# Kernel tuning notes

Hardware: AMD Instinct MI355X
Metric: run time of the kernel (lower is better)

Reference implementation:

```python
import jax, jax.numpy as jnp
import numpy as np

B, T, C, H = 2, 2048, 1024, 16
D = C // H  # head_dim = 64


def setup_inputs() -> dict:
    key = jax.random.key(0)
    ks = jax.random.split(key, 5)
    s = 1.0 / np.sqrt(C)
    return {
        "x": jax.random.normal(ks[0], (B, T, C), jnp.float32),
        "Wq": jax.random.normal(ks[1], (C, C), jnp.float32) * s,
        "bq": jnp.zeros((C,), jnp.float32),
        "Wk": jax.random.normal(ks[2], (C, C), jnp.float32) * s,
        "bk": jnp.zeros((C,), jnp.float32),
        "Wv": jax.random.normal(ks[3], (C, C), jnp.float32) * s,
        "bv": jnp.zeros((C,), jnp.float32),
        "Wo": jax.random.normal(ks[4], (C, C), jnp.float32) * s,
        "bo": jnp.zeros((C,), jnp.float32),
    }


def reference(x, Wq, bq, Wk, bk, Wv, bv, Wo, bo):
    Bx, Tx, Cx = x.shape
    # torch Linear: y = x @ W.T + b
    q = (x @ Wq.T + bq).reshape(Bx, Tx, H, D).transpose(0, 2, 1, 3)  # [B,H,T,D]
    k = (x @ Wk.T + bk).reshape(Bx, Tx, H, D).transpose(0, 2, 1, 3)
    v = (x @ Wv.T + bv).reshape(Bx, Tx, H, D).transpose(0, 2, 1, 3)
    att = jnp.einsum("bhqd,bhkd->bhqk", q, k) / np.sqrt(D).astype(np.float32)
    mask = jnp.tril(jnp.ones((Tx, Tx), bool))  # causal mask [T,T]
    att = jnp.where(mask, att, -jnp.inf)
    att = jax.nn.softmax(att, axis=-1)
    out = jnp.einsum("bhqk,bhkd->bhqd", att, v)
    out = out.transpose(0, 2, 1, 3).reshape(Bx, Tx, Cx)
    return out @ Wo.T + bo
```

## Files before the change

kernel.cpp:

```cpp
#include <hip/hip_runtime.h>
#include <hip/hip_bf16.h>

#define B_ 2
#define T_ 2048
#define C_ 1024
#define H_ 16
#define D_ 64

typedef unsigned short u16;
typedef __bf16 bf16x8 __attribute__((ext_vector_type(8)));
typedef float floatx4 __attribute__((ext_vector_type(4)));

__device__ __forceinline__ float bf2f(u16 u) {
  union { unsigned int i; float f; } x; x.i = ((unsigned int)u) << 16; return x.f;
}
__device__ __forceinline__ u16 f2bf(float f) {
  union { float f; unsigned int i; } x; x.f = f;
  unsigned int r = x.i + 0x7fffu + ((x.i >> 16) & 1u);
  return (u16)(r >> 16);
}

__device__ __forceinline__ unsigned cvtpk(float lo, float hi) {
  unsigned r;
  asm("v_cvt_pk_bf16_f32 %0, %1, %2" : "=v"(r) : "v"(lo), "v"(hi));
  return r;
}

__device__ __forceinline__ void gld16(void* lds, const void* g) {
  __builtin_amdgcn_global_load_lds(
      (const __attribute__((address_space(1))) unsigned int*)g,
      (__attribute__((address_space(3))) unsigned int*)lds, 16, 0, 0);
}

#define NXF4 1048576
#define NWF4 262144

__global__ __launch_bounds__(256) void cvt_all(
    const float* __restrict__ x,  const float* __restrict__ Wq,
    const float* __restrict__ Wk, const float* __restrict__ Wv,
    const float* __restrict__ Wo, u16* __restrict__ dst_base)
{
  const int i = blockIdx.x * 256 + threadIdx.x;
  const float* src; size_t off;
  if (i < NXF4)               { src = x;  off = i; }
  else if (i < NXF4 + NWF4)   { src = Wq; off = i - NXF4; }
  else if (i < NXF4 + 2*NWF4) { src = Wk; off = i - (NXF4 + NWF4); }
  else if (i < NXF4 + 3*NWF4) { src = Wv; off = i - (NXF4 + 2*NWF4); }
  else                        { src = Wo; off = i - (NXF4 + 3*NWF4); }
  float4 f = ((const float4*)src)[off];
  ushort4 o;
  o.x = f2bf(f.x); o.y = f2bf(f.y); o.z = f2bf(f.z); o.w = f2bf(f.w);
  ((ushort4*)dst_base)[i] = o;
}

#define QSCALE 0.1803368801111f

#define PBAR()                                                \
  do {                                                        \
    asm volatile("" ::: "memory");                            \
    __builtin_amdgcn_s_barrier();                             \
    asm volatile("s_waitcnt lgkmcnt(0)" ::: "memory");        \
  } while (0)

#define EBAR()                                                \
  do {                                                        \
    asm volatile("" ::: "memory");                            \
    __builtin_amdgcn_s_barrier();                             \
    asm volatile("" ::: "memory");                            \
  } while (0)

__global__ __launch_bounds__(512, 2) void gemm_qkv8(
    const u16* __restrict__ X, const u16* __restrict__ Wb,
    const float* __restrict__ b0, const float* __restrict__ b1,
    const float* __restrict__ b2,
    u16* __restrict__ Yq, u16* __restrict__ Yk, u16* __restrict__ Yv)
{
  __shared__ __align__(16) u16 L[57344];

  const int tid  = threadIdx.x;
  const int lane = tid & 63;
  const int m16  = lane & 15;
  const int q4   = lane >> 4;
  const int wv   = tid >> 6;
  const int wm   = wv >> 2;
  const int wn   = wv & 3;

  const int bid = blockIdx.x;
  const int xcd = bid & 7;
  const int idx = bid >> 3;
  const int bx  = (xcd & 3) * 4 + (idx & 3);
  const int by  = (xcd >> 2) * 8 + (idx >> 2);

  const u16* Abase  = X  + (size_t)bx * 256 * C_;
  const u16* Bbase  = Wb + (size_t)by * 192 * C_;
  const u16* A1base = Abase + (size_t)128 * C_;

  const int rB  = tid >> 3;
  const int s0 = tid,       r0 = rB;
  const int s1 = tid + 512, r1 = 64 + rB;
  const int k0a = ((tid & 7) ^ (rB & 7)) * 8;

#define STAGE_A(dsthalf, srcrows, kofs)                                       \
  do {                                                                        \
    gld16(&(dsthalf)[s0 * 8], (srcrows) + (size_t)r0 * C_ + (kofs) + k0a);    \
    gld16(&(dsthalf)[s1 * 8], (srcrows) + (size_t)r1 * C_ + (kofs) + k0a);    \
  } while (0)

#define STAGE_BL(dstB, srcrows, kofs, l)                                      \
  gld16(&(dstB)[((l) * 512 + tid) * 8],                                       \
        (srcrows) + (size_t)((l) * 64 + rB) * C_ + (kofs) + k0a)

  u16* buf0 = L;
  u16* buf1 = L + 28672;

  STAGE_BL(buf0 + 16384, Bbase, 0, 0);
  STAGE_BL(buf0 + 16384, Bbase, 0, 1);
  STAGE_BL(buf0 + 16384, Bbase, 0, 2);
  STAGE_A (buf0,         Abase,  0);
  STAGE_A (buf0 + 8192,  A1base, 0);
  STAGE_BL(buf1 + 16384, Bbase, 64, 0);
  STAGE_BL(buf1 + 16384, Bbase, 64, 1);
  STAGE_A (buf1,         Abase, 64);
  asm volatile("s_waitcnt vmcnt(4)" ::: "memory");
  __builtin_amdgcn_s_barrier();
  asm volatile("" ::: "memory");

  floatx4 acc[8][3] = {};

  const int a0off = m16 * 64 + ((q4      ^ (lane & 7)) * 8);
  const int a1off = m16 * 64 + (((q4 + 4) ^ (lane & 7)) * 8);
  const int bro   = wn * 3072;

  for (int i = 0; i < 16; ++i) {
    u16* buf  = (i & 1) ? buf1 : buf0;
    u16* bufn = (i & 1) ? buf0 : buf1;
    const u16* Ah = buf + wm * 8192;
    const u16* Bh = buf + 16384;
    const bool p1 = (i + 1) < 16;
    const bool p2 = (i + 2) < 16;
    const int  k1 = (i + 1) * 64;
    const int  k2 = (i + 2) * 64;

    bf16x8 a[4][2], bA[2][2], bB[2];

#pragma unroll
    for (int f = 0; f < 4; ++f) {
      a[f][0] = *(const bf16x8*)&Ah[f * 1024 + a0off];
      a[f][1] = *(const bf16x8*)&Ah[f * 1024 + a1off];
    }
#pragma unroll
    for (int g = 0; g < 2; ++g) {
      bA[g][0] = *(const bf16x8*)&Bh[bro + g * 1024 + a0off];
      bA[g][1] = *(const bf16x8*)&Bh[bro + g * 1024 + a1off];
    }
    if (p1) STAGE_A(bufn + 8192, A1base, k1);
    PBAR();
    __builtin_amdgcn_s_setprio(1);
#pragma unroll
    for (int f = 0; f < 4; ++f)
#pragma unroll
      for (int g = 0; g < 2; ++g) {
        acc[f][g] = __builtin_amdgcn_mfma_f32_16x16x32_bf16(a[f][0], bA[g][0], acc[f][g], 0, 0, 0);
        acc[f][g] = __builtin_amdgcn_mfma_f32_16x16x32_bf16(a[f][1], bA[g][1], acc[f][g], 0, 0, 0);
      }
    __builtin_amdgcn_s_setprio(0);
    EBAR();

    bB[0] = *(const bf16x8*)&Bh[bro + 2048 + a0off];
    bB[1] = *(const bf16x8*)&Bh[bro + 2048 + a1off];
    if (p1) STAGE_BL(bufn + 16384, Bbase, k1, 2);
    PBAR();
    __builtin_amdgcn_s_setprio(1);
#pragma unroll
    for (int f = 0; f < 4; ++f) {
      acc[f][2] = __builtin_amdgcn_mfma_f32_16x16x32_bf16(a[f][0], bB[0], acc[f][2], 0, 0, 0);
      acc[f][2] = __builtin_amdgcn_mfma_f32_16x16x32_bf16(a[f][1], bB[1], acc[f][2], 0, 0, 0);
    }
    __builtin_amdgcn_s_setprio(0);
    EBAR();

#pragma unroll
    for (int f = 0; f < 4; ++f) {
      a[f][0] = *(const bf16x8*)&Ah[4096 + f * 1024 + a0off];
      a[f][1] = *(const bf16x8*)&Ah[4096 + f * 1024 + a1off];
    }
    if (p2) {
      STAGE_BL(buf + 16384, Bbase, k2, 0);
      STAGE_BL(buf + 16384, Bbase, k2, 1);
    }
    PBAR();
    __builtin_amdgcn_s_setprio(1);
#pragma unroll
    for (int f = 0; f < 4; ++f) {
      acc[4 + f][2] = __builtin_amdgcn_mfma_f32_16x16x32_bf16(a[f][0], bB[0], acc[4 + f][2], 0, 0, 0);
      acc[4 + f][2] = __builtin_amdgcn_mfma_f32_16x16x32_bf16(a[f][1], bB[1], acc[4 + f][2], 0, 0, 0);
    }
    __builtin_amdgcn_s_setprio(0);
    EBAR();

    if (p2) STAGE_A(buf, Abase, k2);
    PBAR();
    __builtin_amdgcn_s_setprio(1);
#pragma unroll
    for (int f = 0; f < 4; ++f)
#pragma unroll
      for (int g = 0; g < 2; ++g) {
        acc[4 + f][g] = __builtin_amdgcn_mfma_f32_16x16x32_bf16(a[f][0], bA[g][0], acc[4 + f][g], 0, 0, 0);
        acc[4 + f][g] = __builtin_amdgcn_mfma_f32_16x16x32_bf16(a[f][1], bA[g][1], acc[4 + f][g], 0, 0, 0);
      }
    __builtin_amdgcn_s_setprio(0);
    asm volatile("" ::: "memory");
    if (p2) asm volatile("s_waitcnt vmcnt(4)" ::: "memory");
    else    asm volatile("s_waitcnt vmcnt(0)" ::: "memory");
    __builtin_amdgcn_s_barrier();
    asm volatile("" ::: "memory");
  }

  const int mbase = bx * 256 + wm * 128 + q4 * 4;
#pragma unroll
  for (int nf = 0; nf < 3; ++nf) {
    const int nzg = by * 192 + wn * 48 + nf * 16 + m16;
    const int z  = nzg >> 10;
    const int nl = nzg & 1023;
    if (z == 2) {
      const int h = nl >> 6, d = nl & (D_ - 1);
      const float bv = b2[nl];
#pragma unroll
      for (int mf = 0; mf < 8; ++mf) {
        const int m  = mbase + mf * 16;
        const int bb = m >> 11, t = m & (T_ - 1);
        ushort4 pk;
        pk.x = f2bf(acc[mf][nf][0] + bv);
        pk.y = f2bf(acc[mf][nf][1] + bv);
        pk.z = f2bf(acc[mf][nf][2] + bv);
        pk.w = f2bf(acc[mf][nf][3] + bv);
        *(ushort4*)&Yv[(((size_t)bb * H_ + h) * D_ + d) * T_ + t] = pk;
      }
    } else {
      const float bv = (z == 0 ? b0 : b1)[nl];
      const float sc = z ? 1.0f : QSCALE;
      const int c_loc = wn * 48 + nf * 16 + m16;
      const int chunk = c_loc >> 3, cl = c_loc & 7;
#pragma unroll
      for (int mf = 0; mf < 8; ++mf) {
#pragma unroll
        for (int r = 0; r < 4; ++r) {
          const int t_loc = wm * 128 + mf * 16 + q4 * 4 + r;
          const int pc = ((chunk & ~7) | ((chunk & 7) ^ (t_loc & 7))) * 8 + cl;
          L[t_loc * 192 + pc] = f2bf((acc[mf][nf][r] + bv) * sc);
        }
      }
    }
  }
  __syncthreads();
  {
    const int row_off = tid >> 3;
    const int ch_off  = tid & 7;
#pragma unroll
    for (int gi = 0; gi < 3; ++gi) {
      const int gg = by * 3 + gi;
      const int z  = gg >> 4;
      if (z == 2) continue;
      u16* Y = z ? Yk : Yq;
      const int h = gg & 15;
#pragma unroll
      for (int pass = 0; pass < 4; ++pass) {
        const int t_loc = pass * 64 + row_off;
        const int pl3 = ch_off ^ (t_loc & 7);
        const uint4 val = *(const uint4*)&L[t_loc * 192 + (gi * 8 + pl3) * 8];
        const int m = bx * 256 + t_loc;
        const int bb = m >> 11, tq = m & (T_ - 1);
        *(uint4*)&Y[(((size_t)bb * H_ + h) * T_ + tq) * D_ + ch_off * 8] = val;
      }
    }
  }
}

__global__ __launch_bounds__(256) void gemm_out(
    const u16* __restrict__ X, const u16* __restrict__ W,
    const float* __restrict__ bias, float* __restrict__ Yf)
{
  const int K = C_, N = C_;
  __shared__ __align__(16) u16 As[128 * 32];
  __shared__ __align__(16) u16 Bs[128 * 32];

  const int tid  = threadIdx.x;
  const int wv   = tid >> 6;
  const int lane = tid & 63;
  const int mcol = lane & 15;
  const int quad = lane >> 4;
  const int wr = wv >> 1, wc = wv & 1;
  const int m0 = blockIdx.x * 128;
  const int n0 = blockIdx.y * 128;

  const int srow = tid >> 2;
  const int scol = (tid & 3) * 8;
  const u16* xp0 = X + (size_t)(m0 + srow) * K + scol;
  const u16* xp1 = xp0 + (size_t)64 * K;
  const u16* wp0 = W + (size_t)(n0 + srow) * K + scol;
  const u16* wp1 = wp0 + (size_t)64 * K;

  floatx4 acc[4][4] = {};

  for (int k0 = 0; k0 < K; k0 += 32) {
    gld16(&As[tid * 8],        xp0 + k0);
    gld16(&As[2048 + tid * 8], xp1 + k0);
    gld16(&Bs[tid * 8],        wp0 + k0);
    gld16(&Bs[2048 + tid * 8], wp1 + k0);
    __syncthreads();

    bf16x8 a[4], b[4];
#pragma unroll
    for (int rf = 0; rf < 4; ++rf)
      a[rf] = *(const bf16x8*)&As[(wr * 64 + rf * 16 + mcol) * 32 + quad * 8];
#pragma unroll
    for (int cf = 0; cf < 4; ++cf)
      b[cf] = *(const bf16x8*)&Bs[(wc * 64 + cf * 16 + mcol) * 32 + quad * 8];
#pragma unroll
    for (int rf = 0; rf < 4; ++rf)
#pragma unroll
      for (int cf = 0; cf < 4; ++cf)
        acc[rf][cf] = __builtin_amdgcn_mfma_f32_16x16x32_bf16(
            a[rf], b[cf], acc[rf][cf], 0, 0, 0);
    __syncthreads();
  }

#pragma unroll
  for (int cf = 0; cf < 4; ++cf) {
    const int n = n0 + wc * 64 + cf * 16 + mcol;
    const float bv = bias[n];
#pragma unroll
    for (int rf = 0; rf < 4; ++rf) {
#pragma unroll
      for (int r = 0; r < 4; ++r) {
        const int m = m0 + wr * 64 + rf * 16 + quad * 4 + r;
        Yf[(size_t)m * N + n] = acc[rf][cf][r] + bv;
      }
    }
  }
}

#define KSB 4096
#define VTB 4096

__constant__ unsigned char CH_T[24]  = {7,15,15,14,14,6,13,13, 4,10,10,5,11,11,12,12, 9,9,8,8,3,2,1,0};
__constant__ unsigned char CH_J0[24] = {0,0,16,0,15,0,0,14,   0,0,11,0,0,12,0,13,    0,10,0,9,0,0,0,0};
__constant__ unsigned char CH_J1[24] = {15,15,31,14,29,13,13,27, 9,10,21,11,11,23,12,25, 9,19,8,17,7,5,3,1};
__constant__ unsigned char CH_P[24]  = {0,1,2,1,2,0,1,2,      0,1,2,0,1,2,1,2,       1,2,1,2,0,0,0,0};

__global__ __launch_bounds__(256, 3) void attn_flash(
    const u16* __restrict__ Q, const u16* __restrict__ K,
    const u16* __restrict__ Vg, u16* __restrict__ O,
    float* __restrict__ OP, float* __restrict__ LP)
{
  __shared__ __align__(16) u16 Ks[3 * KSB];
  __shared__ __align__(16) u16 Vt[3 * VTB];

  const int tid  = threadIdx.x;
  const int wv   = tid >> 6;
  const int lane = tid & 63;
  const int mcol = lane & 15;
  const int quad = lane >> 4;

  const int bx = blockIdx.x;
  const int bh = bx & 31;
  const int c  = bx >> 5;
  const int t  = CH_T[c];
  const int j0 = CH_J0[c];
  const int j1 = CH_J1[c];
  const int pm = CH_P[c];
  const int ti = pm ? ((bh * 8 + (t - 8)) * 2 + (pm - 1)) : 0;

  const size_t base  = (size_t)bh * T_ * D_;
  const size_t vbase = (size_t)bh * D_ * T_;
  const int b = bh >> 4, h = bh & (H_ - 1);

  bf16x8 vones;
  {
    const u16 ov = (mcol == 0) ? (u16)0x3F80 : (u16)0;
    union { u16 s[8]; bf16x8 v; } tmp;
#pragma unroll
    for (int i = 0; i < 8; ++i) tmp.s[i] = ov;
    vones = tmp.v;
  }

  const int srow = lane >> 3;
  const int sg   = (lane & 7) ^ srow;
  const int c0 = wv * 2, c1 = wv * 2 + 1;
  const int sl0 = (quad ^ (mcol & 7)) * 8;

  const size_t koff0 = base + (size_t)(c0 * 8 + srow) * D_ + sg * 8;
  const size_t koff1 = base + (size_t)(c1 * 8 + srow) * D_ + sg * 8;
  const size_t voff0 = vbase + (size_t)(c0 * 8 + srow) * T_ + sg * 8;
  const size_t voff1 = vbase + (size_t)(c1 * 8 + srow) * T_ + sg * 8;

  const u16* qg = Q + base + (size_t)(t * 128 + wv * 32 + mcol) * D_ + quad * 8;
  const bf16x8 qf[2][2] = {
    { *(const bf16x8*)qg,             *(const bf16x8*)(qg + 32) },
    { *(const bf16x8*)(qg + 16 * D_), *(const bf16x8*)(qg + 16 * D_ + 32) }
  };

  floatx4 oacc[2][5] = {};

#define STG_KV(bufi, jt)                                                      \
  do {                                                                        \
    const size_t kj_ = (size_t)(jt) * 64 * D_;                                \
    const int    vj_ = (jt) * 64;                                             \
    gld16(&Ks[(bufi) * KSB + c0 * 512 + lane * 8], K  + koff0 + kj_);         \
    gld16(&Ks[(bufi) * KSB + c1 * 512 + lane * 8], K  + koff1 + kj_);         \
    gld16(&Vt[(bufi) * VTB + c0 * 512 + lane * 8], Vg + voff0 + vj_);         \
    gld16(&Vt[(bufi) * VTB + c1 * 512 + lane * 8], Vg + voff1 + vj_);         \
  } while (0)

  STG_KV(0, j0);
  if (j0 + 1 <= j1) STG_KV(1, j0 + 1);

  int cur = 0;
  for (int j = j0; j <= j1; ++j) {
    asm volatile("" ::: "memory");
    if (j < j1) asm volatile("s_waitcnt vmcnt(4)" ::: "memory");
    else        asm volatile("s_waitcnt vmcnt(0)" ::: "memory");
    __builtin_amdgcn_s_barrier();
    asm volatile("" ::: "memory");

    if (j + 2 <= j1) {
      int nb = cur + 2; if (nb >= 3) nb -= 3;
      STG_KV(nb, j + 2);
    }

    const u16* ksb = &Ks[cur * KSB];
    const u16* vtb = &Vt[cur * VTB];

    floatx4 sacc[2][4] = {};
    __builtin_amdgcn_s_setprio(1);
#pragma unroll
    for (int nt = 0; nt < 4; ++nt) {
      const u16* kr = &ksb[(nt * 16 + mcol) * 64];
      bf16x8 kb0 = *(const bf16x8*)&kr[sl0];
      bf16x8 kb1 = *(const bf16x8*)&kr[sl0 ^ 32];
      sacc[0][nt] = __builtin_amdgcn_mfma_f32_16x16x32_bf16(kb0, qf[0][0], sacc[0][nt], 0, 0, 0);
      sacc[0][nt] = __builtin_amdgcn_mfma_f32_16x16x32_bf16(kb1, qf[0][1], sacc[0][nt], 0, 0, 0);
      sacc[1][nt] = __builtin_amdgcn_mfma_f32_16x16x32_bf16(kb0, qf[1][0], sacc[1][nt], 0, 0, 0);
      sacc[1][nt] = __builtin_amdgcn_mfma_f32_16x16x32_bf16(kb1, qf[1][1], sacc[1][nt], 0, 0, 0);
    }
    __builtin_amdgcn_s_setprio(0);

    const int dj = j - 2 * t;
    if (dj >= 0) {
#pragma unroll
      for (int hf = 0; hf < 2; ++hf) {
        const int klim = wv * 32 + hf * 16 + mcol - dj * 64;
#pragma unroll
        for (int nt = 0; nt < 4; ++nt)
#pragma unroll
          for (int r = 0; r < 4; ++r)
            if (nt * 16 + quad * 4 + r > klim) sacc[hf][nt][r] = -1e30f;
      }
    }

    bf16x8 pa[2][2];
#pragma unroll
    for (int hf = 0; hf < 2; ++hf) {
      unsigned w[4][2];
#pragma unroll
      for (int nt = 0; nt < 4; ++nt)
#pragma unroll
        for (int i = 0; i < 2; ++i)
          w[nt][i] = cvtpk(exp2f(sacc[hf][nt][2*i]), exp2f(sacc[hf][nt][2*i+1]));
      union { unsigned u[4]; bf16x8 v; } p0, p1;
#pragma unroll
      for (int i = 0; i < 2; ++i) {
        unsigned x = w[0][i], y = w[1][i];
        asm("v_permlane32_swap_b32 %0, %1" : "+v"(x), "+v"(y));
        asm("v_permlane16_swap_b32 %0, %1" : "+v"(x), "+v"(y));
        p0.u[i] = x; p0.u[i + 2] = y;
        unsigned x2 = w[2][i], y2 = w[3][i];
        asm("v_permlane32_swap_b32 %0, %1" : "+v"(x2), "+v"(y2));
        asm("v_permlane16_swap_b32 %0, %1" : "+v"(x2), "+v"(y2));
        p1.u[i] = x2; p1.u[i + 2] = y2;
      }
      pa[hf][0] = p0.v; pa[hf][1] = p1.v;
    }

    __builtin_amdgcn_s_setprio(1);
#pragma unroll
    for (int dt = 0; dt < 4; ++dt) {
      const u16* vr = &vtb[(dt * 16 + mcol) * 64];
      bf16x8 vb0 = *(const bf16x8*)&vr[sl0];
      bf16x8 vb1 = *(const bf16x8*)&vr[sl0 ^ 32];
      oacc[0][dt] = __builtin_amdgcn_mfma_f32_16x16x32_bf16(pa[0][0], vb0, oacc[0][dt], 0, 0, 0);
      oacc[0][dt] = __builtin_amdgcn_mfma_f32_16x16x32_bf16(pa[0][1], vb1, oacc[0][dt], 0, 0, 0);
      oacc[1][dt] = __builtin_amdgcn_mfma_f32_16x16x32_bf16(pa[1][0], vb0, oacc[1][dt], 0, 0, 0);
      oacc[1][dt] = __builtin_amdgcn_mfma_f32_16x16x32_bf16(pa[1][1], vb1, oacc[1][dt], 0, 0, 0);
    }
    oacc[0][4] = __builtin_amdgcn_mfma_f32_16x16x32_bf16(pa[0][0], vones, oacc[0][4], 0, 0, 0);
    oacc[0][4] = __builtin_amdgcn_mfma_f32_16x16x32_bf16(pa[0][1], vones, oacc[0][4], 0, 0, 0);
    oacc[1][4] = __builtin_amdgcn_mfma_f32_16x16x32_bf16(pa[1][0], vones, oacc[1][4], 0, 0, 0);
    oacc[1][4] = __builtin_amdgcn_mfma_f32_16x16x32_bf16(pa[1][1], vones, oacc[1][4], 0, 0, 0);
    __builtin_amdgcn_s_setprio(0);

    cur = (cur == 2) ? 0 : cur + 1;
  }

  if (!pm) {
#pragma unroll
    for (int hf = 0; hf < 2; ++hf) {
      float invl[4];
#pragma unroll
      for (int r = 0; r < 4; ++r)
        invl[r] = 1.f / __shfl(oacc[hf][4][r], lane & 48);
#pragma unroll
      for (int dt = 0; dt < 4; ++dt) {
        const int cc = h * D_ + dt * 16 + mcol;
#pragma unroll
        for (int r = 0; r < 4; ++r) {
          const int tg = t * 128 + wv * 32 + hf * 16 + quad * 4 + r;
          O[((size_t)b * T_ + tg) * C_ + cc] = f2bf(oacc[hf][dt][r] * invl[r]);
        }
      }
    }
  } else {
    float* op = OP + (size_t)ti * 8192;
#pragma unroll
    for (int hf = 0; hf < 2; ++hf) {
#pragma unroll
      for (int dt = 0; dt < 4; ++dt)
#pragma unroll
        for (int r = 0; r < 4; ++r)
          op[(wv * 32 + hf * 16 + quad * 4 + r) * 64 + dt * 16 + mcol] = oacc[hf][dt][r];
      if (mcol == 0) {
#pragma unroll
        for (int r = 0; r < 4; ++r)
          LP[ti * 128 + wv * 32 + hf * 16 + quad * 4 + r] = oacc[hf][4][r];
      }
    }
  }
}

__global__ __launch_bounds__(256) void attn_merge(
    const float* __restrict__ OP, const float* __restrict__ LP,
    u16* __restrict__ O)
{
  const int mb = blockIdx.x;
  const int bh = mb & 31, tt = mb >> 5;
  const int t = 8 + tt;
  const int ti0 = (bh * 8 + tt) * 2;
  const int b = bh >> 4, h = bh & (H_ - 1);
  const int row = threadIdx.x >> 1;
  const int dc  = (threadIdx.x & 1) * 32;

  const float l = LP[ti0 * 128 + row] + LP[(ti0 + 1) * 128 + row];
  const float inv = 1.f / l;
  const float* pa = OP + (size_t)ti0 * 8192 + row * 64 + dc;
  const float* pb = pa + 8192;

  const int tg = t * 128 + row;
  u16* o = O + ((size_t)b * T_ + tg) * C_ + h * D_ + dc;

  u16 tmp[32];
#pragma unroll
  for (int i = 0; i < 8; ++i) {
    const float4 a4 = ((const float4*)pa)[i];
    const float4 b4 = ((const float4*)pb)[i];
    tmp[i*4 + 0] = f2bf((a4.x + b4.x) * inv);
    tmp[i*4 + 1] = f2bf((a4.y + b4.y) * inv);
    tmp[i*4 + 2] = f2bf((a4.z + b4.z) * inv);
    tmp[i*4 + 3] = f2bf((a4.w + b4.w) * inv);
  }
#pragma unroll
  for (int i = 0; i < 4; ++i)
    ((uint4*)o)[i] = ((const uint4*)tmp)[i];
}

extern "C" void kernel_launch(void* const* d_in, const int* in_sizes, int n_in,
                              void* d_out, int out_size, void* d_ws, size_t ws_size,
                              hipStream_t stream) {
  const float* x  = (const float*)d_in[0];
  const float* Wq = (const float*)d_in[1];
  const float* bq = (const float*)d_in[2];
  const float* Wk = (const float*)d_in[3];
  const float* bk = (const float*)d_in[4];
  const float* Wv = (const float*)d_in[5];
  const float* bv = (const float*)d_in[6];
  const float* Wo = (const float*)d_in[7];
  const float* bo = (const float*)d_in[8];
  float* out = (float*)d_out;

  const size_t NX = (size_t)B_ * T_ * C_;
  const size_t NW = (size_t)C_ * C_;

  u16* xb  = (u16*)d_ws;
  u16* wqb = xb  + NX;
  u16* wkb = wqb + NW;
  u16* wvb = wkb + NW;
  u16* wob = wvb + NW;
  u16* q   = wob + NW;
  u16* k   = q   + NX;
  u16* v   = k   + NX;
  u16* ctx = v   + NX;
  float* opart = (float*)(ctx + NX);
  float* lpart = opart + (size_t)512 * 8192;

  cvt_all<<<dim3((NXF4 + 4 * NWF4) / 256), 256, 0, stream>>>(x, Wq, Wk, Wv, Wo, xb);

  gemm_qkv8<<<dim3(256), 512, 0, stream>>>(xb, wqb, bq, bk, bv, q, k, v);

  attn_flash<<<dim3(768), 256, 0, stream>>>(q, k, v, ctx, opart, lpart);

  attn_merge<<<dim3(256), 256, 0, stream>>>(opart, lpart, ctx);

  gemm_out<<<dim3(32, 8), 256, 0, stream>>>(ctx, wob, bo, out);
}
```

Before: 183.8 us.

## Halve QKV GEMM M-tile to 128 rows, doubling grid and occupancy

The fused QKV projection GEMM now uses a 128x192 output tile instead of 256x192. This halves the LDS footprint and the accumulator registers per block and doubles the grid from 256 to 512 blocks, so launch bounds can allow more resident blocks per CU. The staging pipeline and XCD-aware block mapping are reworked for the smaller A tile. The cost is less reuse of each B (weight) tile per block, which means more global and L2 traffic for the weights.

```diff
diff --git a/kernel.cpp b/kernel.cpp
--- a/kernel.cpp
+++ b/kernel.cpp
@@ -69,13 +69,13 @@
     asm volatile("" ::: "memory");                            \
   } while (0)
 
-__global__ __launch_bounds__(512, 2) void gemm_qkv8(
+__global__ __launch_bounds__(512, 4) void gemm_qkv8(
     const u16* __restrict__ X, const u16* __restrict__ Wb,
     const float* __restrict__ b0, const float* __restrict__ b1,
     const float* __restrict__ b2,
     u16* __restrict__ Yq, u16* __restrict__ Yk, u16* __restrict__ Yv)
 {
-  __shared__ __align__(16) u16 L[57344];
+  __shared__ __align__(16) u16 L[40960];
 
   const int tid  = threadIdx.x;
   const int lane = tid & 63;
@@ -88,54 +88,43 @@
   const int bid = blockIdx.x;
   const int xcd = bid & 7;
   const int idx = bid >> 3;
-  const int bx  = (xcd & 3) * 4 + (idx & 3);
-  const int by  = (xcd >> 2) * 8 + (idx >> 2);
-
-  const u16* Abase  = X  + (size_t)bx * 256 * C_;
-  const u16* Bbase  = Wb + (size_t)by * 192 * C_;
-  const u16* A1base = Abase + (size_t)128 * C_;
+  const int bx  = (xcd & 3) * 8 + (idx & 7);
+  const int by  = (xcd >> 2) * 8 + (idx >> 3);
+
+  const u16* Abase = X  + (size_t)bx * 128 * C_;
+  const u16* Bbase = Wb + (size_t)by * 192 * C_;
 
   const int rB  = tid >> 3;
-  const int s0 = tid,       r0 = rB;
-  const int s1 = tid + 512, r1 = 64 + rB;
   const int k0a = ((tid & 7) ^ (rB & 7)) * 8;
 
-#define STAGE_A(dsthalf, srcrows, kofs)                                       \
-  do {                                                                        \
-    gld16(&(dsthalf)[s0 * 8], (srcrows) + (size_t)r0 * C_ + (kofs) + k0a);    \
-    gld16(&(dsthalf)[s1 * 8], (srcrows) + (size_t)r1 * C_ + (kofs) + k0a);    \
-  } while (0)
-
-#define STAGE_BL(dstB, srcrows, kofs, l)                                      \
-  gld16(&(dstB)[((l) * 512 + tid) * 8],                                       \
-        (srcrows) + (size_t)((l) * 64 + rB) * C_ + (kofs) + k0a)
+#define STG_U(dst, srcrows, unit, kofs)                                       \
+  gld16(&(dst)[((unit) * 512 + tid) * 8],                                     \
+        (srcrows) + (size_t)((unit) * 64 + rB) * C_ + (kofs) + k0a)
 
   u16* buf0 = L;
-  u16* buf1 = L + 28672;
-
-  STAGE_BL(buf0 + 16384, Bbase, 0, 0);
-  STAGE_BL(buf0 + 16384, Bbase, 0, 1);
-  STAGE_BL(buf0 + 16384, Bbase, 0, 2);
-  STAGE_A (buf0,         Abase,  0);
-  STAGE_A (buf0 + 8192,  A1base, 0);
-  STAGE_BL(buf1 + 16384, Bbase, 64, 0);
-  STAGE_BL(buf1 + 16384, Bbase, 64, 1);
-  STAGE_A (buf1,         Abase, 64);
-  asm volatile("s_waitcnt vmcnt(4)" ::: "memory");
+  u16* buf1 = L + 20480;
+
+  STG_U(buf0 + 8192, Bbase, 0, 0);
+  STG_U(buf0 + 8192, Bbase, 1, 0);
+  STG_U(buf0 + 8192, Bbase, 2, 0);
+  STG_U(buf0,        Abase, 0, 0);
+  STG_U(buf0,        Abase, 1, 0);
+  STG_U(buf1 + 8192, Bbase, 0, 64);
+  STG_U(buf1 + 8192, Bbase, 1, 64);
+  asm volatile("s_waitcnt vmcnt(2)" ::: "memory");
   __builtin_amdgcn_s_barrier();
   asm volatile("" ::: "memory");
 
-  floatx4 acc[8][3] = {};
+  floatx4 acc[4][3] = {};
 
   const int a0off = m16 * 64 + ((q4      ^ (lane & 7)) * 8);
   const int a1off = m16 * 64 + (((q4 + 4) ^ (lane & 7)) * 8);
-  const int bro   = wn * 3072;
+  const int aro   = wm * 4096;
+  const int bro   = 8192 + wn * 3072;
 
   for (int i = 0; i < 16; ++i) {
     u16* buf  = (i & 1) ? buf1 : buf0;
     u16* bufn = (i & 1) ? buf0 : buf1;
-    const u16* Ah = buf + wm * 8192;
-    const u16* Bh = buf + 16384;
     const bool p1 = (i + 1) < 16;
     const bool p2 = (i + 2) < 16;
     const int  k1 = (i + 1) * 64;
@@ -144,20 +133,20 @@
     bf16x8 a[4][2], bA[2][2], bB[2];
 
 #pragma unroll
-    for (int f = 0; f < 4; ++f) {
-      a[f][0] = *(const bf16x8*)&Ah[f * 1024 + a0off];
-      a[f][1] = *(const bf16x8*)&Ah[f * 1024 + a1off];
+    for (int f = 0; f < 2; ++f) {
+      a[f][0] = *(const bf16x8*)&buf[aro + f * 1024 + a0off];
+      a[f][1] = *(const bf16x8*)&buf[aro + f * 1024 + a1off];
     }
 #pragma unroll
     for (int g = 0; g < 2; ++g) {
-      bA[g][0] = *(const bf16x8*)&Bh[bro + g * 1024 + a0off];
-      bA[g][1] = *(const bf16x8*)&Bh[bro + g * 1024 + a1off];
-    }
-    if (p1) STAGE_A(bufn + 8192, A1base, k1);
+      bA[g][0] = *(const bf16x8*)&buf[bro + g * 1024 + a0off];
+      bA[g][1] = *(const bf16x8*)&buf[bro + g * 1024 + a1off];
+    }
+    if (p1) { STG_U(bufn, Abase, 0, k1); STG_U(bufn, Abase, 1, k1); }
     PBAR();
     __builtin_amdgcn_s_setprio(1);
 #pragma unroll
-    for (int f = 0; f < 4; ++f)
+    for (int f = 0; f < 2; ++f)
 #pragma unroll
       for (int g = 0; g < 2; ++g) {
         acc[f][g] = __builtin_amdgcn_mfma_f32_16x16x32_bf16(a[f][0], bA[g][0], acc[f][g], 0, 0, 0);
@@ -166,13 +155,13 @@
     __builtin_amdgcn_s_setprio(0);
     EBAR();
 
-    bB[0] = *(const bf16x8*)&Bh[bro + 2048 + a0off];
-    bB[1] = *(const bf16x8*)&Bh[bro + 2048 + a1off];
-    if (p1) STAGE_BL(bufn + 16384, Bbase, k1, 2);
+    bB[0] = *(const bf16x8*)&buf[bro + 2048 + a0off];
+    bB[1] = *(const bf16x8*)&buf[bro + 2048 + a1off];
+    if (p1) STG_U(bufn + 8192, Bbase, 2, k1);
     PBAR();
     __builtin_amdgcn_s_setprio(1);
 #pragma unroll
-    for (int f = 0; f < 4; ++f) {
+    for (int f = 0; f < 2; ++f) {
       acc[f][2] = __builtin_amdgcn_mfma_f32_16x16x32_bf16(a[f][0], bB[0], acc[f][2], 0, 0, 0);
       acc[f][2] = __builtin_amdgcn_mfma_f32_16x16x32_bf16(a[f][1], bB[1], acc[f][2], 0, 0, 0);
     }
@@ -180,43 +169,42 @@
     EBAR();
 
 #pragma unroll
-    for (int f = 0; f < 4; ++f) {
-      a[f][0] = *(const bf16x8*)&Ah[4096 + f * 1024 + a0off];
-      a[f][1] = *(const bf16x8*)&Ah[4096 + f * 1024 + a1off];
+    for (int f = 2; f < 4; ++f) {
+      a[f][0] = *(const bf16x8*)&buf[aro + f * 1024 + a0off];
+      a[f][1] = *(const bf16x8*)&buf[aro + f * 1024 + a1off];
     }
     if (p2) {
-      STAGE_BL(buf + 16384, Bbase, k2, 0);
-      STAGE_BL(buf + 16384, Bbase, k2, 1);
+      STG_U(buf + 8192, Bbase, 0, k2);
+      STG_U(buf + 8192, Bbase, 1, k2);
     }
     PBAR();
     __builtin_amdgcn_s_setprio(1);
 #pragma unroll
-    for (int f = 0; f < 4; ++f) {
-      acc[4 + f][2] = __builtin_amdgcn_mfma_f32_16x16x32_bf16(a[f][0], bB[0], acc[4 + f][2], 0, 0, 0);
-      acc[4 + f][2] = __builtin_amdgcn_mfma_f32_16x16x32_bf16(a[f][1], bB[1], acc[4 + f][2], 0, 0, 0);
+    for (int f = 2; f < 4; ++f) {
+      acc[f][2] = __builtin_amdgcn_mfma_f32_16x16x32_bf16(a[f][0], bB[0], acc[f][2], 0, 0, 0);
+      acc[f][2] = __builtin_amdgcn_mfma_f32_16x16x32_bf16(a[f][1], bB[1], acc[f][2], 0, 0, 0);
     }
     __builtin_amdgcn_s_setprio(0);
     EBAR();
 
-    if (p2) STAGE_A(buf, Abase, k2);
     PBAR();
     __builtin_amdgcn_s_setprio(1);
 #pragma unroll
-    for (int f = 0; f < 4; ++f)
+    for (int f = 2; f < 4; ++f)
 #pragma unroll
       for (int g = 0; g < 2; ++g) {
-        acc[4 + f][g] = __builtin_amdgcn_mfma_f32_16x16x32_bf16(a[f][0], bA[g][0], acc[4 + f][g], 0, 0, 0);
-        acc[4 + f][g] = __builtin_amdgcn_mfma_f32_16x16x32_bf16(a[f][1], bA[g][1], acc[4 + f][g], 0, 0, 0);
+        acc[f][g] = __builtin_amdgcn_mfma_f32_16x16x32_bf16(a[f][0], bA[g][0], acc[f][g], 0, 0, 0);
+        acc[f][g] = __builtin_amdgcn_mfma_f32_16x16x32_bf16(a[f][1], bA[g][1], acc[f][g], 0, 0, 0);
       }
     __builtin_amdgcn_s_setprio(0);
     asm volatile("" ::: "memory");
-    if (p2) asm volatile("s_waitcnt vmcnt(4)" ::: "memory");
+    if (p2) asm volatile("s_waitcnt vmcnt(2)" ::: "memory");
     else    asm volatile("s_waitcnt vmcnt(0)" ::: "memory");
     __builtin_amdgcn_s_barrier();
     asm volatile("" ::: "memory");
   }
 
-  const int mbase = bx * 256 + wm * 128 + q4 * 4;
+  const int mbase = bx * 128 + wm * 64 + q4 * 4;
 #pragma unroll
   for (int nf = 0; nf < 3; ++nf) {
     const int nzg = by * 192 + wn * 48 + nf * 16 + m16;
@@ -226,14 +214,14 @@
       const int h = nl >> 6, d = nl & (D_ - 1);
       const float bv = b2[nl];
 #pragma unroll
-      for (int mf = 0; mf < 8; ++mf) {
-        const int m  = mbase + mf * 16;
+      for (int rf = 0; rf < 4; ++rf) {
+        const int m  = mbase + rf * 16;
         const int bb = m >> 11, t = m & (T_ - 1);
         ushort4 pk;
-        pk.x = f2bf(acc[mf][nf][0] + bv);
-        pk.y = f2bf(acc[mf][nf][1] + bv);
-        pk.z = f2bf(acc[mf][nf][2] + bv);
-        pk.w = f2bf(acc[mf][nf][3] + bv);
+        pk.x = f2bf(acc[rf][nf][0] + bv);
+        pk.y = f2bf(acc[rf][nf][1] + bv);
+        pk.z = f2bf(acc[rf][nf][2] + bv);
+        pk.w = f2bf(acc[rf][nf][3] + bv);
         *(ushort4*)&Yv[(((size_t)bb * H_ + h) * D_ + d) * T_ + t] = pk;
       }
     } else {
@@ -242,12 +230,12 @@
       const int c_loc = wn * 48 + nf * 16 + m16;
       const int chunk = c_loc >> 3, cl = c_loc & 7;
 #pragma unroll
-      for (int mf = 0; mf < 8; ++mf) {
+      for (int rf = 0; rf < 4; ++rf) {
 #pragma unroll
         for (int r = 0; r < 4; ++r) {
-          const int t_loc = wm * 128 + mf * 16 + q4 * 4 + r;
+          const int t_loc = wm * 64 + rf * 16 + q4 * 4 + r;
           const int pc = ((chunk & ~7) | ((chunk & 7) ^ (t_loc & 7))) * 8 + cl;
-          L[t_loc * 192 + pc] = f2bf((acc[mf][nf][r] + bv) * sc);
+          L[t_loc * 192 + pc] = f2bf((acc[rf][nf][r] + bv) * sc);
         }
       }
     }
@@ -264,11 +252,11 @@
       u16* Y = z ? Yk : Yq;
       const int h = gg & 15;
 #pragma unroll
-      for (int pass = 0; pass < 4; ++pass) {
+      for (int pass = 0; pass < 2; ++pass) {
         const int t_loc = pass * 64 + row_off;
         const int pl3 = ch_off ^ (t_loc & 7);
         const uint4 val = *(const uint4*)&L[t_loc * 192 + (gi * 8 + pl3) * 8];
-        const int m = bx * 256 + t_loc;
+        const int m = bx * 128 + t_loc;
         const int bb = m >> 11, tq = m & (T_ - 1);
         *(uint4*)&Y[(((size_t)bb * H_ + h) * T_ + tq) * D_ + ch_off * 8] = val;
       }
@@ -603,7 +591,7 @@
 
   cvt_all<<<dim3((NXF4 + 4 * NWF4) / 256), 256, 0, stream>>>(x, Wq, Wk, Wv, Wo, xb);
 
-  gemm_qkv8<<<dim3(256), 512, 0, stream>>>(xb, wqb, bq, bk, bv, q, k, v);
+  gemm_qkv8<<<dim3(512), 512, 0, stream>>>(xb, wqb, bq, bk, bv, q, k, v);
 
   attn_flash<<<dim3(768), 256, 0, stream>>>(q, k, v, ctx, opart, lpart);
 
```

Result: no change. 180.8 us (median of 2 runs) (-1.6%).
